# Kernel optimization log

Hardware: AMD Instinct MI355X
Metric: run time of the kernel (lower is better)

Reference implementation:

```python
import jax, jax.numpy as jnp
import numpy as np

B, N, L, H, V, OV, MAX_STEPS = 16, 256, 4, 128, 512, 1000, 48


def setup_inputs() -> dict:
    key = jax.random.key(0)
    ks = jax.random.split(key, 20)
    s = lambda fan_in: 1.0 / np.sqrt(fan_in)
    return {
        'data': jax.random.randint(ks[0], (B, N, L), 0, V, dtype=jnp.int32),
        'true_branch_nodes': jax.random.randint(ks[1], (B, N), 0, N, dtype=jnp.int32),
        'false_branch_nodes': jax.random.randint(ks[2], (B, N), 0, N, dtype=jnp.int32),
        'start_index': jax.random.randint(ks[3], (B,), 0, N, dtype=jnp.int32),
        'exit_index': jax.random.randint(ks[4], (B,), 0, N, dtype=jnp.int32),
        'steps': jax.random.randint(ks[5], (B,), 1, MAX_STEPS + 1, dtype=jnp.int32),
        'embed_w': jax.random.uniform(ks[6], (V, H), jnp.float32, -0.1, 0.1),
        'Wi0': jax.random.normal(ks[7], (H, 4 * H), jnp.float32) * s(H),
        'Wh0': jax.random.normal(ks[8], (H, 4 * H), jnp.float32) * s(H),
        'b0': jnp.zeros((4 * H,), jnp.float32),
        'Wi1': jax.random.normal(ks[9], (H, 4 * H), jnp.float32) * s(H),
        'Wh1': jax.random.normal(ks[10], (H, 4 * H), jnp.float32) * s(H),
        'b1': jnp.zeros((4 * H,), jnp.float32),
        'branch_w': jax.random.normal(ks[11], (4 * H, 2), jnp.float32) * s(4 * H),
        'branch_b': jax.random.normal(ks[12], (2,), jnp.float32) * 1e-6,
        'out_w': jax.random.normal(ks[13], (H, OV), jnp.float32) * s(H),
        'out_b': jax.random.normal(ks[14], (OV,), jnp.float32) * 1e-6,
    }


def _lstm(c, h, x, Wi, Wh, b):
    # flax LSTMCell gate order: i, f, g, o
    z = x @ Wi + h @ Wh + b
    i, f, g, o = jnp.split(z, 4, axis=-1)
    c = jax.nn.sigmoid(f) * c + jax.nn.sigmoid(i) * jnp.tanh(g)
    h = jax.nn.sigmoid(o) * jnp.tanh(c)
    return c, h


def reference(data, true_branch_nodes, false_branch_nodes, start_index, exit_index, steps,
              embed_w, Wi0, Wh0, b0, Wi1, Wh1, b1, branch_w, branch_b, out_w, out_b):
    num_nodes = data.shape[1]

    def single_example(data_e, true_idx, false_idx, start, exit_i, n_steps):
        emb_t = jnp.swapaxes(embed_w[data_e], 0, 1)  # [L, N, H]
        hs0 = tuple(jnp.zeros((num_nodes, H), embed_w.dtype) for _ in range(4))  # (c0,h0,c1,h1)
        ip0 = jnp.zeros((num_nodes,), embed_w.dtype).at[start].set(1.0)

        def execute(hs):
            # run 2-layer stacked LSTM over each node's statement tokens (vectorized over nodes)
            def tok_step(carry, x):
                c0, h0, c1, h1 = carry
                c0, h0 = _lstm(c0, h0, x, Wi0, Wh0, b0)
                c1, h1 = _lstm(c1, h1, h0, Wi1, Wh1, b1)
                return (c0, h0, c1, h1), None
            carry, _ = jax.lax.scan(tok_step, hs, emb_t)
            return carry

        def step(carry, idx):
            hs, ip = carry
            contrib = execute(hs)
            # exit node keeps its previous hidden state
            contrib = tuple(c.at[exit_i].set(h[exit_i]) for c, h in zip(contrib, hs))
            concat = jnp.concatenate(contrib, axis=-1)  # [N, 4H]
            p = jax.nn.softmax(concat @ branch_w + branch_b, axis=-1)
            pt, pf = p[:, 0], p[:, 1]
            wt, wf = pt * ip, pf * ip
            ip_new = (jax.ops.segment_sum(wt, true_idx, num_segments=num_nodes)
                      + jax.ops.segment_sum(wf, false_idx, num_segments=num_nodes))
            denom = (ip_new + 1e-7)[:, None]
            def agg(hleaf):
                t = jax.ops.segment_sum(hleaf * wt[:, None], true_idx, num_segments=num_nodes)
                f = jax.ops.segment_sum(hleaf * wf[:, None], false_idx, num_segments=num_nodes)
                return (t + f) / denom
            hs_new = tuple(agg(hleaf) for hleaf in contrib)
            active = idx < n_steps
            hs = tuple(jnp.where(active, new, old) for new, old in zip(hs_new, hs))
            ip = jnp.where(active, ip_new, ip)
            return (hs, ip), None

        (hs, ip), _ = jax.lax.scan(step, (hs0, ip0), jnp.arange(MAX_STEPS))
        return hs[3][exit_i] @ out_w + out_b  # top-layer h at exit node -> [OV]

    return jax.vmap(single_example)(data, true_branch_nodes, false_branch_nodes,
                                    start_index, exit_index, steps)
```

## Files before the change

### kernel.cpp

```cpp
#include <hip/hip_runtime.h>

namespace {
constexpr int B = 16, N = 256, L = 4, H = 128, V = 512, OV = 1000, MAX_STEPS = 48;
constexpr int Z = 4 * H;
constexpr int BN = B * N;
constexpr int PADK = 132;
}

typedef __attribute__((ext_vector_type(8))) short short8;
typedef __attribute__((ext_vector_type(4))) short short4v;
typedef __attribute__((ext_vector_type(4))) float f32x4;

__device__ __forceinline__ float sigf(float x) { return 1.0f / (1.0f + __expf(-x)); }
__device__ __forceinline__ float tanh_f(float x) { return 1.0f - 2.0f / (__expf(2.0f * x) + 1.0f); }

__device__ __forceinline__ unsigned short bf16_rne(float x) {
    unsigned u = __float_as_uint(x);
    return (unsigned short)((u + 0x7fffu + ((u >> 16) & 1u)) >> 16);
}
__device__ __forceinline__ void split2(float x, unsigned short& hi, unsigned short& lo) {
    hi = bf16_rne(x);
    const float hf = __uint_as_float(((unsigned)hi) << 16);
    lo = bf16_rne(x - hf);
}

__device__ __forceinline__ short8 ldsA(const unsigned short* p) {
    const short4v a = *(const short4v*)p;
    const short4v b = *(const short4v*)(p + 16);
    return __builtin_shufflevector(a, b, 0, 1, 2, 3, 4, 5, 6, 7);
}

__global__ __launch_bounds__(256) void k_init(float4* __restrict__ cur4,
                                              float* __restrict__ ip,
                                              const int* __restrict__ start) {
    const int idx = blockIdx.x * 256 + threadIdx.x;
    cur4[idx] = make_float4(0.f, 0.f, 0.f, 0.f);
    if (idx < BN) ip[idx] = ((idx & (N - 1)) == start[idx >> 8]) ? 1.0f : 0.0f;
}

__global__ __launch_bounds__(256) void k_tokz(const float* __restrict__ emb,
                                              const float* __restrict__ Wi0,
                                              const float* __restrict__ b0,
                                              float* __restrict__ tokz) {
    __shared__ float lds_a[16 * 128];
    float4* l4 = (float4*)lds_a;
    const int tid = threadIdx.x;
    const int c = tid & 127, rg = tid >> 7;
    const int row0 = blockIdx.x * 16;
    {
        const float4* a4 = (const float4*)emb;
        l4[tid] = a4[row0 * 32 + tid];
        l4[tid + 256] = a4[row0 * 32 + tid + 256];
    }
    __syncthreads();
    float acc[8][4];
    {
        float bq[4];
#pragma unroll
        for (int q = 0; q < 4; q++) bq[q] = b0[c + q * 128];
#pragma unroll
        for (int i = 0; i < 8; i++)
#pragma unroll
            for (int q = 0; q < 4; q++) acc[i][q] = bq[q];
    }
    for (int k4 = 0; k4 < 32; k4++) {
        float4 a[8];
#pragma unroll
        for (int i = 0; i < 8; i++) a[i] = l4[(rg * 8 + i) * 32 + k4];
#pragma unroll
        for (int j = 0; j < 4; j++) {
            const int k = k4 * 4 + j;
            const float* wr = Wi0 + k * Z + c;
            const float w0 = wr[0], w1 = wr[128], w2 = wr[256], w3 = wr[384];
#pragma unroll
            for (int i = 0; i < 8; i++) {
                const float av = (j == 0) ? a[i].x : (j == 1) ? a[i].y : (j == 2) ? a[i].z : a[i].w;
                acc[i][0] += av * w0;
                acc[i][1] += av * w1;
                acc[i][2] += av * w2;
                acc[i][3] += av * w3;
            }
        }
    }
#pragma unroll
    for (int i = 0; i < 8; i++) {
        const int row = row0 + rg * 8 + i;
#pragma unroll
        for (int q = 0; q < 4; q++) tokz[row * Z + c + q * 128] = acc[i][q];
    }
}

__global__ __launch_bounds__(256) void k_pack(const float* __restrict__ Wh0,
                                              const float* __restrict__ Wi1,
                                              const float* __restrict__ Wh1,
                                              unsigned short* __restrict__ WPhi,
                                              unsigned short* __restrict__ WPlo) {
    const int gid = blockIdx.x * 256 + threadIdx.x;
    const int lp = gid & 63;
    const int ks = (gid >> 6) & 3;
    const int w = (gid >> 8) & 7;
    const int q = (gid >> 11) & 3;
    const int split = (gid >> 13) & 1;
    const int mat = gid >> 14;
    const float* W = (mat == 0) ? Wh0 : (mat == 1) ? Wi1 : Wh1;
    const int g = lp >> 4, li = lp & 15;
    const int col = q * 128 + w * 16 + li;
    const int e = ((mat * 4 + q) * 8 + w) * 4 + ks;
    unsigned short* dst = (split ? WPlo : WPhi) + (size_t)e * 512 + lp * 8;
#pragma unroll
    for (int j = 0; j < 8; j++) {
        const int k = ks * 32 + ((j & 4) ? 16 : 0) + g * 4 + (j & 3);
        const float x = W[k * Z + col];
        const unsigned short hi = bf16_rne(x);
        unsigned short v = hi;
        if (split) {
            const float hf = __uint_as_float(((unsigned)hi) << 16);
            v = bf16_rne(x - hf);
        }
        dst[j] = v;
    }
}

__global__ __launch_bounds__(256) void k_csr(const int* __restrict__ tix,
                                             const int* __restrict__ fix,
                                             int* __restrict__ off,
                                             int* __restrict__ ent) {
    const int b = blockIdx.x;
    const int m = threadIdx.x;
    __shared__ int cnt[N];
    __shared__ int wsum[4];
    cnt[m] = 0;
    __syncthreads();
    const int ti = tix[b * N + m];
    const int fi = fix[b * N + m];
    atomicAdd(&cnt[ti], 1);
    atomicAdd(&cnt[fi], 1);
    __syncthreads();
    const int v = cnt[m];
    const int lane = m & 63, w = m >> 6;
    int sc = v;
#pragma unroll
    for (int o = 1; o < 64; o <<= 1) {
        const int t = __shfl_up(sc, o);
        if (lane >= o) sc += t;
    }
    if (lane == 63) wsum[w] = sc;
    __syncthreads();
    int add = 0;
    for (int i = 0; i < w; i++) add += wsum[i];
    const int base = sc - v + add;
    off[b * (N + 1) + m] = base;
    if (m == N - 1) off[b * (N + 1) + N] = base + v;
    __syncthreads();
    cnt[m] = base;
    __syncthreads();
    const int p1 = atomicAdd(&cnt[ti], 1);
    ent[b * 2 * N + p1] = (m << 1);
    const int p2 = atomicAdd(&cnt[fi], 1);
    ent[b * 2 * N + p2] = (m << 1) | 1;
}

__global__ __launch_bounds__(512) void k_scan(
    const float* __restrict__ c0c, const float* __restrict__ h0c,
    const float* __restrict__ c1c, const float* __restrict__ h1c,
    float* __restrict__ c0w, float* __restrict__ h0w,
    float* __restrict__ c1w, float* __restrict__ h1w,
    const unsigned short* __restrict__ WPhi, const unsigned short* __restrict__ WPlo,
    const float* __restrict__ b1,
    const float* __restrict__ tokz, const int* __restrict__ data,
    const float* __restrict__ bw, const float* __restrict__ bb,
    const float* __restrict__ ip, float* __restrict__ wt, float* __restrict__ wf,
    const int* __restrict__ exiti, const int* __restrict__ steps, const int s) {
    const int bx = blockIdx.x;
    const int b = bx >> 4;
    if (s >= steps[b]) return;
    const int row0 = bx * 16;
    const int tid = threadIdx.x;
    const int w = tid >> 6;
    const int l = tid & 63;
    const int g = l >> 4, li = l & 15;
    const int ch = w * 16 + li;

    __shared__ unsigned short h0hi[16 * PADK], h0lo[16 * PADK];
    __shared__ unsigned short h1hi[16 * PADK], h1lo[16 * PADK];
    __shared__ float red[16][8][2];

    float c0[4], c1[4], h0[4], h1[4];
#pragma unroll
    for (int r = 0; r < 4; r++) {
        const int off = (row0 + g * 4 + r) * H + ch;
        c0[r] = c0c[off];
        h0[r] = h0c[off];
        c1[r] = c1c[off];
        h1[r] = h1c[off];
    }
    float b1v[4];
#pragma unroll
    for (int q = 0; q < 4; q++) b1v[q] = b1[q * 128 + ch];

#pragma unroll
    for (int r = 0; r < 4; r++) {
        unsigned short hi, lo;
        split2(h0[r], hi, lo);
        h0hi[(g * 4 + r) * PADK + ch] = hi;
        h0lo[(g * 4 + r) * PADK + ch] = lo;
        split2(h1[r], hi, lo);
        h1hi[(g * 4 + r) * PADK + ch] = hi;
        h1lo[(g * 4 + r) * PADK + ch] = lo;
    }
    __syncthreads();

#pragma unroll 1
    for (int t = 0; t < L; t++) {
        f32x4 acc[4];
        {
            int tok[4];
#pragma unroll
            for (int r = 0; r < 4; r++) tok[r] = data[(row0 + g * 4 + r) * L + t];
#pragma unroll
            for (int q = 0; q < 4; q++)
#pragma unroll
                for (int r = 0; r < 4; r++) acc[q][r] = tokz[tok[r] * Z + q * 128 + ch];
        }
#pragma unroll
        for (int q = 0; q < 4; q++) {
#pragma unroll
            for (int ks = 0; ks < 4; ks++) {
                const int ab = li * PADK + ks * 32 + g * 4;
                const short8 ahi = ldsA(&h0hi[ab]);
                const short8 alo = ldsA(&h0lo[ab]);
                const int e = (q * 8 + w) * 4 + ks;
                const short8 bhi = *(const short8*)(WPhi + (size_t)e * 512 + l * 8);
                const short8 blo = *(const short8*)(WPlo + (size_t)e * 512 + l * 8);
                acc[q] = __builtin_amdgcn_mfma_f32_16x16x32_bf16(ahi, bhi, acc[q], 0, 0, 0);
                acc[q] = __builtin_amdgcn_mfma_f32_16x16x32_bf16(ahi, blo, acc[q], 0, 0, 0);
                acc[q] = __builtin_amdgcn_mfma_f32_16x16x32_bf16(alo, bhi, acc[q], 0, 0, 0);
            }
            __builtin_amdgcn_sched_barrier(0);
        }
#pragma unroll
        for (int r = 0; r < 4; r++) {
            const float cn = sigf(acc[1][r]) * c0[r] + sigf(acc[0][r]) * tanh_f(acc[2][r]);
            c0[r] = cn;
            h0[r] = sigf(acc[3][r]) * tanh_f(cn);
        }
        __syncthreads();
#pragma unroll
        for (int r = 0; r < 4; r++) {
            unsigned short hi, lo;
            split2(h0[r], hi, lo);
            h0hi[(g * 4 + r) * PADK + ch] = hi;
            h0lo[(g * 4 + r) * PADK + ch] = lo;
        }
        __syncthreads();
#pragma unroll
        for (int q = 0; q < 4; q++) {
            const float bv = b1v[q];
            acc[q][0] = bv; acc[q][1] = bv; acc[q][2] = bv; acc[q][3] = bv;
        }
#pragma unroll
        for (int q = 0; q < 4; q++) {
#pragma unroll
            for (int ks = 0; ks < 4; ks++) {
                const int ab = li * PADK + ks * 32 + g * 4;
                const short8 a0hi = ldsA(&h0hi[ab]);
                const short8 a0lo = ldsA(&h0lo[ab]);
                const short8 a1hi = ldsA(&h1hi[ab]);
                const short8 a1lo = ldsA(&h1lo[ab]);
                const int e1 = ((4 + q) * 8 + w) * 4 + ks;
                const int e2 = ((8 + q) * 8 + w) * 4 + ks;
                const short8 b1hi = *(const short8*)(WPhi + (size_t)e1 * 512 + l * 8);
                const short8 b1lo = *(const short8*)(WPlo + (size_t)e1 * 512 + l * 8);
                const short8 b2hi = *(const short8*)(WPhi + (size_t)e2 * 512 + l * 8);
                const short8 b2lo = *(const short8*)(WPlo + (size_t)e2 * 512 + l * 8);
                acc[q] = __builtin_amdgcn_mfma_f32_16x16x32_bf16(a0hi, b1hi, acc[q], 0, 0, 0);
                acc[q] = __builtin_amdgcn_mfma_f32_16x16x32_bf16(a0hi, b1lo, acc[q], 0, 0, 0);
                acc[q] = __builtin_amdgcn_mfma_f32_16x16x32_bf16(a0lo, b1hi, acc[q], 0, 0, 0);
                acc[q] = __builtin_amdgcn_mfma_f32_16x16x32_bf16(a1hi, b2hi, acc[q], 0, 0, 0);
                acc[q] = __builtin_amdgcn_mfma_f32_16x16x32_bf16(a1hi, b2lo, acc[q], 0, 0, 0);
                acc[q] = __builtin_amdgcn_mfma_f32_16x16x32_bf16(a1lo, b2hi, acc[q], 0, 0, 0);
            }
            __builtin_amdgcn_sched_barrier(0);
        }
#pragma unroll
        for (int r = 0; r < 4; r++) {
            const float cn = sigf(acc[1][r]) * c1[r] + sigf(acc[0][r]) * tanh_f(acc[2][r]);
            c1[r] = cn;
            h1[r] = sigf(acc[3][r]) * tanh_f(cn);
        }
        __syncthreads();
#pragma unroll
        for (int r = 0; r < 4; r++) {
            unsigned short hi, lo;
            split2(h1[r], hi, lo);
            h1hi[(g * 4 + r) * PADK + ch] = hi;
            h1lo[(g * 4 + r) * PADK + ch] = lo;
        }
        __syncthreads();
    }

    const int ex = exiti[b];
    if ((ex >> 4) == (bx & 15)) {
        const int rl = ex & 15;
#pragma unroll
        for (int r = 0; r < 4; r++) {
            if (g * 4 + r == rl) {
                const int off = (row0 + rl) * H + ch;
                c0[r] = c0c[off];
                h0[r] = h0c[off];
                c1[r] = c1c[off];
                h1[r] = h1c[off];
            }
        }
    }
#pragma unroll
    for (int r = 0; r < 4; r++) {
        const int off = (row0 + g * 4 + r) * H + ch;
        c0w[off] = c0[r];
        h0w[off] = h0[r];
        c1w[off] = c1[r];
        h1w[off] = h1[r];
    }
    float2 bwv[4];
#pragma unroll
    for (int x = 0; x < 4; x++) bwv[x] = ((const float2*)bw)[x * 128 + ch];
    float l0p[4], l1p[4];
#pragma unroll
    for (int r = 0; r < 4; r++) {
        l0p[r] = c0[r] * bwv[0].x + h0[r] * bwv[1].x + c1[r] * bwv[2].x + h1[r] * bwv[3].x;
        l1p[r] = c0[r] * bwv[0].y + h0[r] * bwv[1].y + c1[r] * bwv[2].y + h1[r] * bwv[3].y;
    }
#pragma unroll
    for (int off = 8; off > 0; off >>= 1)
#pragma unroll
        for (int r = 0; r < 4; r++) {
            l0p[r] += __shfl_xor(l0p[r], off);
            l1p[r] += __shfl_xor(l1p[r], off);
        }
    if (li == 0)
#pragma unroll
        for (int r = 0; r < 4; r++) {
            red[g * 4 + r][w][0] = l0p[r];
            red[g * 4 + r][w][1] = l1p[r];
        }
    __syncthreads();
    if (tid < 16) {
        float l0 = bb[0], l1 = bb[1];
#pragma unroll
        for (int ww = 0; ww < 8; ww++) {
            l0 += red[tid][ww][0];
            l1 += red[tid][ww][1];
        }
        const float m = fmaxf(l0, l1);
        const float e0 = __expf(l0 - m), e1 = __expf(l1 - m);
        const float inv = 1.0f / (e0 + e1);
        const float ipv = ip[row0 + tid];
        wt[row0 + tid] = e0 * inv * ipv;
        wf[row0 + tid] = e1 * inv * ipv;
    }
}

__global__ __launch_bounds__(256) void k_agg(
    const float* __restrict__ c0w, const float* __restrict__ h0w,
    const float* __restrict__ c1w, const float* __restrict__ h1w,
    float* __restrict__ c0c, float* __restrict__ h0c,
    float* __restrict__ c1c, float* __restrict__ h1c,
    const int* __restrict__ off, const int* __restrict__ ent,
    const float* __restrict__ wt, const float* __restrict__ wf,
    float* __restrict__ ip, const int* __restrict__ steps, const int s) {
    const int row00 = blockIdx.x * 4;
    const int b = row00 >> 8;
    if (s >= steps[b]) return;
    const int tid = threadIdx.x;
    const int lane = tid & 63;
    const int n = (row00 & (N - 1)) + (tid >> 6);
    const int rowb = b * N;
    const int beg = off[b * (N + 1) + n];
    const int end = off[b * (N + 1) + n + 1];
    float a00 = 0, a01 = 0, a10 = 0, a11 = 0, a20 = 0, a21 = 0, a30 = 0, a31 = 0;
    float ipacc = 0.f;
    for (int e = beg; e < end; e++) {
        const int pe = ent[b * 2 * N + e];
        const int m = pe >> 1;
        const float wgt = (pe & 1) ? wf[rowb + m] : wt[rowb + m];
        ipacc += wgt;
        const int rb = (rowb + m) * H;
        a00 += c0w[rb + lane] * wgt;
        a01 += c0w[rb + lane + 64] * wgt;
        a10 += h0w[rb + lane] * wgt;
        a11 += h0w[rb + lane + 64] * wgt;
        a20 += c1w[rb + lane] * wgt;
        a21 += c1w[rb + lane + 64] * wgt;
        a30 += h1w[rb + lane] * wgt;
        a31 += h1w[rb + lane + 64] * wgt;
    }
    const float dn = 1.0f / (ipacc + 1e-7f);
    const int ob = (rowb + n) * H;
    c0c[ob + lane] = a00 * dn;
    c0c[ob + lane + 64] = a01 * dn;
    h0c[ob + lane] = a10 * dn;
    h0c[ob + lane + 64] = a11 * dn;
    c1c[ob + lane] = a20 * dn;
    c1c[ob + lane + 64] = a21 * dn;
    h1c[ob + lane] = a30 * dn;
    h1c[ob + lane + 64] = a31 * dn;
    if (lane == 0) ip[rowb + n] = ipacc;
}

__global__ __launch_bounds__(256) void k_out(const float* __restrict__ h1c,
                                             const float* __restrict__ ow,
                                             const float* __restrict__ ob,
                                             const int* __restrict__ exiti,
                                             float* __restrict__ out) {
    const int b = blockIdx.x;
    __shared__ float h[H];
    const int tid = threadIdx.x;
    if (tid < H) h[tid] = h1c[(b * N + exiti[b]) * H + tid];
    __syncthreads();
    for (int v = tid; v < OV; v += 256) {
        float acc = ob[v];
        for (int d = 0; d < H; d++) acc += h[d] * ow[d * OV + v];
        out[b * OV + v] = acc;
    }
}

extern "C" void kernel_launch(void* const* d_in, const int* in_sizes, int n_in,
                              void* d_out, int out_size, void* d_ws, size_t ws_size,
                              hipStream_t stream) {
    (void)in_sizes; (void)n_in; (void)out_size;
    const int* data = (const int*)d_in[0];
    const int* tix = (const int*)d_in[1];
    const int* fix = (const int*)d_in[2];
    const int* start = (const int*)d_in[3];
    const int* exiti = (const int*)d_in[4];
    const int* steps = (const int*)d_in[5];
    const float* emb = (const float*)d_in[6];
    const float* Wi0 = (const float*)d_in[7];
    const float* Wh0 = (const float*)d_in[8];
    const float* b0 = (const float*)d_in[9];
    const float* Wi1 = (const float*)d_in[10];
    const float* Wh1 = (const float*)d_in[11];
    const float* b1 = (const float*)d_in[12];
    const float* bw = (const float*)d_in[13];
    const float* bb = (const float*)d_in[14];
    const float* ow = (const float*)d_in[15];
    const float* obias = (const float*)d_in[16];
    float* out = (float*)d_out;

    const size_t SB = (size_t)BN * H;
    float* ws = (float*)d_ws;
    float* c0c = ws;
    float* h0c = ws + 1 * SB;
    float* c1c = ws + 2 * SB;
    float* h1c = ws + 3 * SB;
    float* c0w = ws + 4 * SB;
    float* h0w = ws + 5 * SB;
    float* c1w = ws + 6 * SB;
    float* h1w = ws + 7 * SB;
    float* tokz = ws + 8 * SB;
    float* ip = tokz + (size_t)V * Z;
    float* wt = ip + BN;
    float* wf = wt + BN;
    unsigned short* WPhi = (unsigned short*)(wf + BN);
    unsigned short* WPlo = WPhi + 3 * 65536;
    int* csr_off = (int*)(WPlo + 3 * 65536);
    int* csr_ent = csr_off + B * (N + 1);
    const size_t need = (8 * SB + (size_t)V * Z + 3 * (size_t)BN) * sizeof(float) +
                        2 * 3 * 65536 * sizeof(unsigned short) +
                        (B * (N + 1) + B * 2 * N) * sizeof(int);
    if (ws_size < need) return;

    k_init<<<(4 * SB / 4) / 256, 256, 0, stream>>>((float4*)ws, ip, start);
    k_tokz<<<V / 16, 256, 0, stream>>>(emb, Wi0, b0, tokz);
    k_pack<<<192, 256, 0, stream>>>(Wh0, Wi1, Wh1, WPhi, WPlo);
    k_csr<<<B, 256, 0, stream>>>(tix, fix, csr_off, csr_ent);

    for (int s = 0; s < MAX_STEPS; s++) {
        k_scan<<<BN / 16, 512, 0, stream>>>(c0c, h0c, c1c, h1c, c0w, h0w, c1w, h1w,
                                            WPhi, WPlo, b1, tokz, data, bw, bb,
                                            ip, wt, wf, exiti, steps, s);
        k_agg<<<BN / 4, 256, 0, stream>>>(c0w, h0w, c1w, h1w, c0c, h0c, c1c, h1c,
                                          csr_off, csr_ent, wt, wf, ip, steps, s);
    }
    k_out<<<B, 256, 0, stream>>>(h1c, ow, obias, exiti, out);
}
```

Baseline: 4.658 ms.

## Fuse segment-sum aggregation into scan kernel with ping-pong work buffers

Removes the separate aggregation and init kernels. Each scan block now gathers its 16 nodes' state from the previous step's ping-pong buffer into LDS, so the current state never round-trips through global memory. The launch count drops from 96 to 49 and the exit-node restore is taken from registers instead of a reload. The trade-offs are a larger LDS footprint per block, which may lower occupancy, and an extra launch at s==MAX_STEPS that writes the final h1.

```diff
diff --git a/kernel.cpp b/kernel.cpp
--- a/kernel.cpp
+++ b/kernel.cpp
@@ -5,6 +5,7 @@
 constexpr int Z = 4 * H;
 constexpr int BN = B * N;
 constexpr int PADK = 132;
+constexpr size_t SB = (size_t)BN * H;
 }
 
 typedef __attribute__((ext_vector_type(8))) short short8;
@@ -28,14 +29,6 @@
     const short4v a = *(const short4v*)p;
     const short4v b = *(const short4v*)(p + 16);
     return __builtin_shufflevector(a, b, 0, 1, 2, 3, 4, 5, 6, 7);
-}
-
-__global__ __launch_bounds__(256) void k_init(float4* __restrict__ cur4,
-                                              float* __restrict__ ip,
-                                              const int* __restrict__ start) {
-    const int idx = blockIdx.x * 256 + threadIdx.x;
-    cur4[idx] = make_float4(0.f, 0.f, 0.f, 0.f);
-    if (idx < BN) ip[idx] = ((idx & (N - 1)) == start[idx >> 8]) ? 1.0f : 0.0f;
 }
 
 __global__ __launch_bounds__(256) void k_tokz(const float* __restrict__ emb,
@@ -161,19 +154,22 @@
 }
 
 __global__ __launch_bounds__(512) void k_scan(
-    const float* __restrict__ c0c, const float* __restrict__ h0c,
-    const float* __restrict__ c1c, const float* __restrict__ h1c,
-    float* __restrict__ c0w, float* __restrict__ h0w,
-    float* __restrict__ c1w, float* __restrict__ h1w,
+    const float* __restrict__ workR,
+    float* __restrict__ workW,
+    const float* __restrict__ wtR, const float* __restrict__ wfR,
+    float* __restrict__ wtW, float* __restrict__ wfW,
+    float* __restrict__ h1c,
     const unsigned short* __restrict__ WPhi, const unsigned short* __restrict__ WPlo,
     const float* __restrict__ b1,
     const float* __restrict__ tokz, const int* __restrict__ data,
     const float* __restrict__ bw, const float* __restrict__ bb,
-    const float* __restrict__ ip, float* __restrict__ wt, float* __restrict__ wf,
-    const int* __restrict__ exiti, const int* __restrict__ steps, const int s) {
+    const int* __restrict__ csr_off, const int* __restrict__ csr_ent,
+    const int* __restrict__ start, const int* __restrict__ exiti,
+    const int* __restrict__ steps, const int s) {
     const int bx = blockIdx.x;
     const int b = bx >> 4;
-    if (s >= steps[b]) return;
+    const int st = steps[b];
+    if (s > st) return;
     const int row0 = bx * 16;
     const int tid = threadIdx.x;
     const int w = tid >> 6;
@@ -184,16 +180,72 @@
     __shared__ unsigned short h0hi[16 * PADK], h0lo[16 * PADK];
     __shared__ unsigned short h1hi[16 * PADK], h1lo[16 * PADK];
     __shared__ float red[16][8][2];
+    __shared__ float curt[4][16][132];
+    __shared__ float ipl[16];
+
+    if (s == 0) {
+        for (int i = tid; i < 4 * 16 * 132; i += 512) (&curt[0][0][0])[i] = 0.f;
+        if (tid < 16) ipl[tid] = ((bx & 15) * 16 + tid == start[b]) ? 1.0f : 0.0f;
+    } else {
+#pragma unroll 1
+        for (int rr = 0; rr < 2; rr++) {
+            const int nloc = w * 2 + rr;
+            const int n = (bx & 15) * 16 + nloc;
+            const int beg = csr_off[b * (N + 1) + n];
+            const int end = csr_off[b * (N + 1) + n + 1];
+            float a00 = 0, a01 = 0, a10 = 0, a11 = 0, a20 = 0, a21 = 0, a30 = 0, a31 = 0;
+            float ipacc = 0.f;
+            for (int e = beg; e < end; e++) {
+                const int pe = csr_ent[b * 2 * N + e];
+                const int m = pe >> 1;
+                const float wgt = (pe & 1) ? wfR[b * N + m] : wtR[b * N + m];
+                ipacc += wgt;
+                const size_t rb = (size_t)(b * N + m) * H;
+                a00 += workR[rb + l] * wgt;
+                a01 += workR[rb + l + 64] * wgt;
+                a10 += workR[SB + rb + l] * wgt;
+                a11 += workR[SB + rb + l + 64] * wgt;
+                a20 += workR[2 * SB + rb + l] * wgt;
+                a21 += workR[2 * SB + rb + l + 64] * wgt;
+                a30 += workR[3 * SB + rb + l] * wgt;
+                a31 += workR[3 * SB + rb + l + 64] * wgt;
+            }
+            const float dn = 1.0f / (ipacc + 1e-7f);
+            curt[0][nloc][l] = a00 * dn;
+            curt[0][nloc][l + 64] = a01 * dn;
+            curt[1][nloc][l] = a10 * dn;
+            curt[1][nloc][l + 64] = a11 * dn;
+            curt[2][nloc][l] = a20 * dn;
+            curt[2][nloc][l + 64] = a21 * dn;
+            curt[3][nloc][l] = a30 * dn;
+            curt[3][nloc][l + 64] = a31 * dn;
+            if (l == 0) ipl[nloc] = ipacc;
+        }
+    }
+    __syncthreads();
 
     float c0[4], c1[4], h0[4], h1[4];
 #pragma unroll
     for (int r = 0; r < 4; r++) {
-        const int off = (row0 + g * 4 + r) * H + ch;
-        c0[r] = c0c[off];
-        h0[r] = h0c[off];
-        c1[r] = c1c[off];
-        h1[r] = h1c[off];
-    }
+        const int rl = g * 4 + r;
+        c0[r] = curt[0][rl][ch];
+        h0[r] = curt[1][rl][ch];
+        c1[r] = curt[2][rl][ch];
+        h1[r] = curt[3][rl][ch];
+    }
+
+    if (s == st) {
+#pragma unroll
+        for (int r = 0; r < 4; r++) h1c[(size_t)(row0 + g * 4 + r) * H + ch] = h1[r];
+        return;
+    }
+
+    const int ex = exiti[b];
+    int rex = -1;
+    if ((ex >> 4) == (bx & 15) && ((ex & 15) >> 2) == g) rex = ex & 3;
+    float sc0 = 0, sh0 = 0, sc1 = 0, sh1 = 0;
+    if (rex >= 0) { sc0 = c0[rex]; sh0 = h0[rex]; sc1 = c1[rex]; sh1 = h1[rex]; }
+
     float b1v[4];
 #pragma unroll
     for (int q = 0; q < 4; q++) b1v[q] = b1[q * 128 + ch];
@@ -299,27 +351,14 @@
         __syncthreads();
     }
 
-    const int ex = exiti[b];
-    if ((ex >> 4) == (bx & 15)) {
-        const int rl = ex & 15;
-#pragma unroll
-        for (int r = 0; r < 4; r++) {
-            if (g * 4 + r == rl) {
-                const int off = (row0 + rl) * H + ch;
-                c0[r] = c0c[off];
-                h0[r] = h0c[off];
-                c1[r] = c1c[off];
-                h1[r] = h1c[off];
-            }
-        }
-    }
+    if (rex >= 0) { c0[rex] = sc0; h0[rex] = sh0; c1[rex] = sc1; h1[rex] = sh1; }
 #pragma unroll
     for (int r = 0; r < 4; r++) {
-        const int off = (row0 + g * 4 + r) * H + ch;
-        c0w[off] = c0[r];
-        h0w[off] = h0[r];
-        c1w[off] = c1[r];
-        h1w[off] = h1[r];
+        const size_t off = (size_t)(row0 + g * 4 + r) * H + ch;
+        workW[off] = c0[r];
+        workW[SB + off] = h0[r];
+        workW[2 * SB + off] = c1[r];
+        workW[3 * SB + off] = h1[r];
     }
     float2 bwv[4];
 #pragma unroll
@@ -354,57 +393,10 @@
         const float m = fmaxf(l0, l1);
         const float e0 = __expf(l0 - m), e1 = __expf(l1 - m);
         const float inv = 1.0f / (e0 + e1);
-        const float ipv = ip[row0 + tid];
-        wt[row0 + tid] = e0 * inv * ipv;
-        wf[row0 + tid] = e1 * inv * ipv;
-    }
-}
-
-__global__ __launch_bounds__(256) void k_agg(
-    const float* __restrict__ c0w, const float* __restrict__ h0w,
-    const float* __restrict__ c1w, const float* __restrict__ h1w,
-    float* __restrict__ c0c, float* __restrict__ h0c,
-    float* __restrict__ c1c, float* __restrict__ h1c,
-    const int* __restrict__ off, const int* __restrict__ ent,
-    const float* __restrict__ wt, const float* __restrict__ wf,
-    float* __restrict__ ip, const int* __restrict__ steps, const int s) {
-    const int row00 = blockIdx.x * 4;
-    const int b = row00 >> 8;
-    if (s >= steps[b]) return;
-    const int tid = threadIdx.x;
-    const int lane = tid & 63;
-    const int n = (row00 & (N - 1)) + (tid >> 6);
-    const int rowb = b * N;
-    const int beg = off[b * (N + 1) + n];
-    const int end = off[b * (N + 1) + n + 1];
-    float a00 = 0, a01 = 0, a10 = 0, a11 = 0, a20 = 0, a21 = 0, a30 = 0, a31 = 0;
-    float ipacc = 0.f;
-    for (int e = beg; e < end; e++) {
-        const int pe = ent[b * 2 * N + e];
-        const int m = pe >> 1;
-        const float wgt = (pe & 1) ? wf[rowb + m] : wt[rowb + m];
-        ipacc += wgt;
-        const int rb = (rowb + m) * H;
-        a00 += c0w[rb + lane] * wgt;
-        a01 += c0w[rb + lane + 64] * wgt;
-        a10 += h0w[rb + lane] * wgt;
-        a11 += h0w[rb + lane + 64] * wgt;
-        a20 += c1w[rb + lane] * wgt;
-        a21 += c1w[rb + lane + 64] * wgt;
-        a30 += h1w[rb + lane] * wgt;
-        a31 += h1w[rb + lane + 64] * wgt;
-    }
-    const float dn = 1.0f / (ipacc + 1e-7f);
-    const int ob = (rowb + n) * H;
-    c0c[ob + lane] = a00 * dn;
-    c0c[ob + lane + 64] = a01 * dn;
-    h0c[ob + lane] = a10 * dn;
-    h0c[ob + lane + 64] = a11 * dn;
-    c1c[ob + lane] = a20 * dn;
-    c1c[ob + lane + 64] = a21 * dn;
-    h1c[ob + lane] = a30 * dn;
-    h1c[ob + lane + 64] = a31 * dn;
-    if (lane == 0) ip[rowb + n] = ipacc;
+        const float ipv = ipl[tid];
+        wtW[row0 + tid] = e0 * inv * ipv;
+        wfW[row0 + tid] = e1 * inv * ipv;
+    }
 }
 
 __global__ __launch_bounds__(256) void k_out(const float* __restrict__ h1c,
@@ -415,7 +407,7 @@
     const int b = blockIdx.x;
     __shared__ float h[H];
     const int tid = threadIdx.x;
-    if (tid < H) h[tid] = h1c[(b * N + exiti[b]) * H + tid];
+    if (tid < H) h[tid] = h1c[(size_t)(b * N + exiti[b]) * H + tid];
     __syncthreads();
     for (int v = tid; v < OV; v += 256) {
         float acc = ob[v];
@@ -447,40 +439,38 @@
     const float* obias = (const float*)d_in[16];
     float* out = (float*)d_out;
 
-    const size_t SB = (size_t)BN * H;
     float* ws = (float*)d_ws;
-    float* c0c = ws;
-    float* h0c = ws + 1 * SB;
-    float* c1c = ws + 2 * SB;
-    float* h1c = ws + 3 * SB;
-    float* c0w = ws + 4 * SB;
-    float* h0w = ws + 5 * SB;
-    float* c1w = ws + 6 * SB;
-    float* h1w = ws + 7 * SB;
-    float* tokz = ws + 8 * SB;
-    float* ip = tokz + (size_t)V * Z;
-    float* wt = ip + BN;
-    float* wf = wt + BN;
-    unsigned short* WPhi = (unsigned short*)(wf + BN);
+    float* tokz = ws;
+    float* work0 = tokz + (size_t)V * Z;
+    float* work1 = work0 + 4 * SB;
+    float* wt0 = work1 + 4 * SB;
+    float* wf0 = wt0 + BN;
+    float* wt1 = wf0 + BN;
+    float* wf1 = wt1 + BN;
+    float* h1c = wf1 + BN;
+    unsigned short* WPhi = (unsigned short*)(h1c + SB);
     unsigned short* WPlo = WPhi + 3 * 65536;
     int* csr_off = (int*)(WPlo + 3 * 65536);
     int* csr_ent = csr_off + B * (N + 1);
-    const size_t need = (8 * SB + (size_t)V * Z + 3 * (size_t)BN) * sizeof(float) +
+    const size_t need = ((size_t)V * Z + 9 * SB + 4 * (size_t)BN) * sizeof(float) +
                         2 * 3 * 65536 * sizeof(unsigned short) +
                         (B * (N + 1) + B * 2 * N) * sizeof(int);
     if (ws_size < need) return;
 
-    k_init<<<(4 * SB / 4) / 256, 256, 0, stream>>>((float4*)ws, ip, start);
     k_tokz<<<V / 16, 256, 0, stream>>>(emb, Wi0, b0, tokz);
     k_pack<<<192, 256, 0, stream>>>(Wh0, Wi1, Wh1, WPhi, WPlo);
     k_csr<<<B, 256, 0, stream>>>(tix, fix, csr_off, csr_ent);
 
-    for (int s = 0; s < MAX_STEPS; s++) {
-        k_scan<<<BN / 16, 512, 0, stream>>>(c0c, h0c, c1c, h1c, c0w, h0w, c1w, h1w,
+    for (int s = 0; s <= MAX_STEPS; s++) {
+        float* workW = (s & 1) ? work1 : work0;
+        const float* workR = (s & 1) ? work0 : work1;
+        float* wtW = (s & 1) ? wt1 : wt0;
+        float* wfW = (s & 1) ? wf1 : wf0;
+        const float* wtR = (s & 1) ? wt0 : wt1;
+        const float* wfR = (s & 1) ? wf0 : wf1;
+        k_scan<<<BN / 16, 512, 0, stream>>>(workR, workW, wtR, wfR, wtW, wfW, h1c,
                                             WPhi, WPlo, b1, tokz, data, bw, bb,
-                                            ip, wt, wf, exiti, steps, s);
-        k_agg<<<BN / 4, 256, 0, stream>>>(c0w, h0w, c1w, h1w, c0c, h0c, c1c, h1c,
-                                          csr_off, csr_ent, wt, wf, ip, steps, s);
+                                            csr_off, csr_ent, start, exiti, steps, s);
     }
     k_out<<<B, 256, 0, stream>>>(h1c, ow, obias, exiti, out);
 }
```

After: 4.819 ms, median of 2. 3.4% more time.

## Process 32 rows per scan block to reuse weight fragments across two MFMA tiles

Applied to the files above, without the earlier changes.

Each k_scan block now handles 32 node rows as two 16-row MFMA tiles, so every weight fragment loaded from global memory feeds two sets of MFMAs. This halves weight traffic per row and halves the block count to 128. Weight loads also switch to nontemporal loads. The trade-offs are fewer blocks on a many-CU GPU, roughly double the accumulator registers, and more shared memory per block.

```diff
diff --git a/kernel.cpp b/kernel.cpp
--- a/kernel.cpp
+++ b/kernel.cpp
@@ -28,6 +28,9 @@
     const short4v a = *(const short4v*)p;
     const short4v b = *(const short4v*)(p + 16);
     return __builtin_shufflevector(a, b, 0, 1, 2, 3, 4, 5, 6, 7);
+}
+__device__ __forceinline__ short8 ldw(const unsigned short* p) {
+    return __builtin_nontemporal_load((const short8*)p);
 }
 
 __global__ __launch_bounds__(256) void k_init(float4* __restrict__ cur4,
@@ -172,179 +175,218 @@
     const float* __restrict__ ip, float* __restrict__ wt, float* __restrict__ wf,
     const int* __restrict__ exiti, const int* __restrict__ steps, const int s) {
     const int bx = blockIdx.x;
-    const int b = bx >> 4;
+    const int b = bx >> 3;
     if (s >= steps[b]) return;
-    const int row0 = bx * 16;
+    const int row0 = bx * 32;
     const int tid = threadIdx.x;
     const int w = tid >> 6;
     const int l = tid & 63;
     const int g = l >> 4, li = l & 15;
     const int ch = w * 16 + li;
 
-    __shared__ unsigned short h0hi[16 * PADK], h0lo[16 * PADK];
-    __shared__ unsigned short h1hi[16 * PADK], h1lo[16 * PADK];
-    __shared__ float red[16][8][2];
-
-    float c0[4], c1[4], h0[4], h1[4];
-#pragma unroll
-    for (int r = 0; r < 4; r++) {
-        const int off = (row0 + g * 4 + r) * H + ch;
-        c0[r] = c0c[off];
-        h0[r] = h0c[off];
-        c1[r] = c1c[off];
-        h1[r] = h1c[off];
-    }
+    __shared__ unsigned short h0hi[32 * PADK], h0lo[32 * PADK];
+    __shared__ unsigned short h1hi[32 * PADK], h1lo[32 * PADK];
+    __shared__ float red[32][8][2];
+
+    float c0[2][4], c1[2][4], h0[2][4], h1[2][4];
+#pragma unroll
+    for (int u = 0; u < 2; u++)
+#pragma unroll
+        for (int r = 0; r < 4; r++) {
+            const int off = (row0 + u * 16 + g * 4 + r) * H + ch;
+            c0[u][r] = c0c[off];
+            h0[u][r] = h0c[off];
+            c1[u][r] = c1c[off];
+            h1[u][r] = h1c[off];
+        }
     float b1v[4];
 #pragma unroll
     for (int q = 0; q < 4; q++) b1v[q] = b1[q * 128 + ch];
 
 #pragma unroll
-    for (int r = 0; r < 4; r++) {
-        unsigned short hi, lo;
-        split2(h0[r], hi, lo);
-        h0hi[(g * 4 + r) * PADK + ch] = hi;
-        h0lo[(g * 4 + r) * PADK + ch] = lo;
-        split2(h1[r], hi, lo);
-        h1hi[(g * 4 + r) * PADK + ch] = hi;
-        h1lo[(g * 4 + r) * PADK + ch] = lo;
-    }
+    for (int u = 0; u < 2; u++)
+#pragma unroll
+        for (int r = 0; r < 4; r++) {
+            const int rl = u * 16 + g * 4 + r;
+            unsigned short hi, lo;
+            split2(h0[u][r], hi, lo);
+            h0hi[rl * PADK + ch] = hi;
+            h0lo[rl * PADK + ch] = lo;
+            split2(h1[u][r], hi, lo);
+            h1hi[rl * PADK + ch] = hi;
+            h1lo[rl * PADK + ch] = lo;
+        }
     __syncthreads();
 
 #pragma unroll 1
     for (int t = 0; t < L; t++) {
-        f32x4 acc[4];
+        f32x4 acc[4][2];
         {
-            int tok[4];
-#pragma unroll
-            for (int r = 0; r < 4; r++) tok[r] = data[(row0 + g * 4 + r) * L + t];
+            int tok[2][4];
+#pragma unroll
+            for (int u = 0; u < 2; u++)
+#pragma unroll
+                for (int r = 0; r < 4; r++)
+                    tok[u][r] = data[(row0 + u * 16 + g * 4 + r) * L + t];
 #pragma unroll
             for (int q = 0; q < 4; q++)
 #pragma unroll
-                for (int r = 0; r < 4; r++) acc[q][r] = tokz[tok[r] * Z + q * 128 + ch];
+                for (int u = 0; u < 2; u++)
+#pragma unroll
+                    for (int r = 0; r < 4; r++)
+                        acc[q][u][r] = tokz[tok[u][r] * Z + q * 128 + ch];
         }
 #pragma unroll
         for (int q = 0; q < 4; q++) {
 #pragma unroll
             for (int ks = 0; ks < 4; ks++) {
-                const int ab = li * PADK + ks * 32 + g * 4;
-                const short8 ahi = ldsA(&h0hi[ab]);
-                const short8 alo = ldsA(&h0lo[ab]);
                 const int e = (q * 8 + w) * 4 + ks;
-                const short8 bhi = *(const short8*)(WPhi + (size_t)e * 512 + l * 8);
-                const short8 blo = *(const short8*)(WPlo + (size_t)e * 512 + l * 8);
-                acc[q] = __builtin_amdgcn_mfma_f32_16x16x32_bf16(ahi, bhi, acc[q], 0, 0, 0);
-                acc[q] = __builtin_amdgcn_mfma_f32_16x16x32_bf16(ahi, blo, acc[q], 0, 0, 0);
-                acc[q] = __builtin_amdgcn_mfma_f32_16x16x32_bf16(alo, bhi, acc[q], 0, 0, 0);
+                const short8 bhi = ldw(WPhi + (size_t)e * 512 + l * 8);
+                const short8 blo = ldw(WPlo + (size_t)e * 512 + l * 8);
+#pragma unroll
+                for (int u = 0; u < 2; u++) {
+                    const int ab = (u * 16 + li) * PADK + ks * 32 + g * 4;
+                    const short8 ahi = ldsA(&h0hi[ab]);
+                    const short8 alo = ldsA(&h0lo[ab]);
+                    acc[q][u] = __builtin_amdgcn_mfma_f32_16x16x32_bf16(ahi, bhi, acc[q][u], 0, 0, 0);
+                    acc[q][u] = __builtin_amdgcn_mfma_f32_16x16x32_bf16(ahi, blo, acc[q][u], 0, 0, 0);
+                    acc[q][u] = __builtin_amdgcn_mfma_f32_16x16x32_bf16(alo, bhi, acc[q][u], 0, 0, 0);
+                }
             }
             __builtin_amdgcn_sched_barrier(0);
         }
 #pragma unroll
-        for (int r = 0; r < 4; r++) {
-            const float cn = sigf(acc[1][r]) * c0[r] + sigf(acc[0][r]) * tanh_f(acc[2][r]);
-            c0[r] = cn;
-            h0[r] = sigf(acc[3][r]) * tanh_f(cn);
-        }
+        for (int u = 0; u < 2; u++)
+#pragma unroll
+            for (int r = 0; r < 4; r++) {
+                const float cn = sigf(acc[1][u][r]) * c0[u][r] + sigf(acc[0][u][r]) * tanh_f(acc[2][u][r]);
+                c0[u][r] = cn;
+                h0[u][r] = sigf(acc[3][u][r]) * tanh_f(cn);
+            }
         __syncthreads();
 #pragma unroll
-        for (int r = 0; r < 4; r++) {
-            unsigned short hi, lo;
-            split2(h0[r], hi, lo);
-            h0hi[(g * 4 + r) * PADK + ch] = hi;
-            h0lo[(g * 4 + r) * PADK + ch] = lo;
-        }
+        for (int u = 0; u < 2; u++)
+#pragma unroll
+            for (int r = 0; r < 4; r++) {
+                const int rl = u * 16 + g * 4 + r;
+                unsigned short hi, lo;
+                split2(h0[u][r], hi, lo);
+                h0hi[rl * PADK + ch] = hi;
+                h0lo[rl * PADK + ch] = lo;
+            }
         __syncthreads();
 #pragma unroll
+        for (int q = 0; q < 4; q++)
+#pragma unroll
+            for (int u = 0; u < 2; u++) {
+                const float bv = b1v[q];
+                acc[q][u][0] = bv; acc[q][u][1] = bv; acc[q][u][2] = bv; acc[q][u][3] = bv;
+            }
+#pragma unroll
         for (int q = 0; q < 4; q++) {
-            const float bv = b1v[q];
-            acc[q][0] = bv; acc[q][1] = bv; acc[q][2] = bv; acc[q][3] = bv;
-        }
-#pragma unroll
-        for (int q = 0; q < 4; q++) {
 #pragma unroll
             for (int ks = 0; ks < 4; ks++) {
-                const int ab = li * PADK + ks * 32 + g * 4;
-                const short8 a0hi = ldsA(&h0hi[ab]);
-                const short8 a0lo = ldsA(&h0lo[ab]);
-                const short8 a1hi = ldsA(&h1hi[ab]);
-                const short8 a1lo = ldsA(&h1lo[ab]);
                 const int e1 = ((4 + q) * 8 + w) * 4 + ks;
                 const int e2 = ((8 + q) * 8 + w) * 4 + ks;
-                const short8 b1hi = *(const short8*)(WPhi + (size_t)e1 * 512 + l * 8);
-                const short8 b1lo = *(const short8*)(WPlo + (size_t)e1 * 512 + l * 8);
-                const short8 b2hi = *(const short8*)(WPhi + (size_t)e2 * 512 + l * 8);
-                const short8 b2lo = *(const short8*)(WPlo + (size_t)e2 * 512 + l * 8);
-                acc[q] = __builtin_amdgcn_mfma_f32_16x16x32_bf16(a0hi, b1hi, acc[q], 0, 0, 0);
-                acc[q] = __builtin_amdgcn_mfma_f32_16x16x32_bf16(a0hi, b1lo, acc[q], 0, 0, 0);
-                acc[q] = __builtin_amdgcn_mfma_f32_16x16x32_bf16(a0lo, b1hi, acc[q], 0, 0, 0);
-                acc[q] = __builtin_amdgcn_mfma_f32_16x16x32_bf16(a1hi, b2hi, acc[q], 0, 0, 0);
-                acc[q] = __builtin_amdgcn_mfma_f32_16x16x32_bf16(a1hi, b2lo, acc[q], 0, 0, 0);
-                acc[q] = __builtin_amdgcn_mfma_f32_16x16x32_bf16(a1lo, b2hi, acc[q], 0, 0, 0);
+                const short8 b1hi = ldw(WPhi + (size_t)e1 * 512 + l * 8);
+                const short8 b1lo = ldw(WPlo + (size_t)e1 * 512 + l * 8);
+                const short8 b2hi = ldw(WPhi + (size_t)e2 * 512 + l * 8);
+                const short8 b2lo = ldw(WPlo + (size_t)e2 * 512 + l * 8);
+#pragma unroll
+                for (int u = 0; u < 2; u++) {
+                    const int ab = (u * 16 + li) * PADK + ks * 32 + g * 4;
+                    const short8 a0hi = ldsA(&h0hi[ab]);
+                    const short8 a0lo = ldsA(&h0lo[ab]);
+                    const short8 a1hi = ldsA(&h1hi[ab]);
+                    const short8 a1lo = ldsA(&h1lo[ab]);
+                    acc[q][u] = __builtin_amdgcn_mfma_f32_16x16x32_bf16(a0hi, b1hi, acc[q][u], 0, 0, 0);
+                    acc[q][u] = __builtin_amdgcn_mfma_f32_16x16x32_bf16(a0hi, b1lo, acc[q][u], 0, 0, 0);
+                    acc[q][u] = __builtin_amdgcn_mfma_f32_16x16x32_bf16(a0lo, b1hi, acc[q][u], 0, 0, 0);
+                    acc[q][u] = __builtin_amdgcn_mfma_f32_16x16x32_bf16(a1hi, b2hi, acc[q][u], 0, 0, 0);
+                    acc[q][u] = __builtin_amdgcn_mfma_f32_16x16x32_bf16(a1hi, b2lo, acc[q][u], 0, 0, 0);
+                    acc[q][u] = __builtin_amdgcn_mfma_f32_16x16x32_bf16(a1lo, b2hi, acc[q][u], 0, 0, 0);
+                }
             }
             __builtin_amdgcn_sched_barrier(0);
         }
 #pragma unroll
+        for (int u = 0; u < 2; u++)
+#pragma unroll
+            for (int r = 0; r < 4; r++) {
+                const float cn = sigf(acc[1][u][r]) * c1[u][r] + sigf(acc[0][u][r]) * tanh_f(acc[2][u][r]);
+                c1[u][r] = cn;
+                h1[u][r] = sigf(acc[3][u][r]) * tanh_f(cn);
+            }
+        __syncthreads();
+#pragma unroll
+        for (int u = 0; u < 2; u++)
+#pragma unroll
+            for (int r = 0; r < 4; r++) {
+                const int rl = u * 16 + g * 4 + r;
+                unsigned short hi, lo;
+                split2(h1[u][r], hi, lo);
+                h1hi[rl * PADK + ch] = hi;
+                h1lo[rl * PADK + ch] = lo;
+            }
+        __syncthreads();
+    }
+
+    const int ex = exiti[b];
+    if ((ex >> 5) == (bx & 7)) {
+        const int rl = ex & 31;
+#pragma unroll
+        for (int u = 0; u < 2; u++)
+#pragma unroll
+            for (int r = 0; r < 4; r++) {
+                if (u * 16 + g * 4 + r == rl) {
+                    const int off = (row0 + rl) * H + ch;
+                    c0[u][r] = c0c[off];
+                    h0[u][r] = h0c[off];
+                    c1[u][r] = c1c[off];
+                    h1[u][r] = h1c[off];
+                }
+            }
+    }
+#pragma unroll
+    for (int u = 0; u < 2; u++)
+#pragma unroll
         for (int r = 0; r < 4; r++) {
-            const float cn = sigf(acc[1][r]) * c1[r] + sigf(acc[0][r]) * tanh_f(acc[2][r]);
-            c1[r] = cn;
-            h1[r] = sigf(acc[3][r]) * tanh_f(cn);
-        }
-        __syncthreads();
+            const int off = (row0 + u * 16 + g * 4 + r) * H + ch;
+            c0w[off] = c0[u][r];
+            h0w[off] = h0[u][r];
+            c1w[off] = c1[u][r];
+            h1w[off] = h1[u][r];
+        }
+    float2 bwv[4];
+#pragma unroll
+    for (int x = 0; x < 4; x++) bwv[x] = ((const float2*)bw)[x * 128 + ch];
+    float l0p[2][4], l1p[2][4];
+#pragma unroll
+    for (int u = 0; u < 2; u++)
 #pragma unroll
         for (int r = 0; r < 4; r++) {
-            unsigned short hi, lo;
-            split2(h1[r], hi, lo);
-            h1hi[(g * 4 + r) * PADK + ch] = hi;
-            h1lo[(g * 4 + r) * PADK + ch] = lo;
-        }
-        __syncthreads();
-    }
-
-    const int ex = exiti[b];
-    if ((ex >> 4) == (bx & 15)) {
-        const int rl = ex & 15;
-#pragma unroll
-        for (int r = 0; r < 4; r++) {
-            if (g * 4 + r == rl) {
-                const int off = (row0 + rl) * H + ch;
-                c0[r] = c0c[off];
-                h0[r] = h0c[off];
-                c1[r] = c1c[off];
-                h1[r] = h1c[off];
-            }
-        }
-    }
-#pragma unroll
-    for (int r = 0; r < 4; r++) {
-        const int off = (row0 + g * 4 + r) * H + ch;
-        c0w[off] = c0[r];
-        h0w[off] = h0[r];
-        c1w[off] = c1[r];
-        h1w[off] = h1[r];
-    }
-    float2 bwv[4];
-#pragma unroll
-    for (int x = 0; x < 4; x++) bwv[x] = ((const float2*)bw)[x * 128 + ch];
-    float l0p[4], l1p[4];
-#pragma unroll
-    for (int r = 0; r < 4; r++) {
-        l0p[r] = c0[r] * bwv[0].x + h0[r] * bwv[1].x + c1[r] * bwv[2].x + h1[r] * bwv[3].x;
-        l1p[r] = c0[r] * bwv[0].y + h0[r] * bwv[1].y + c1[r] * bwv[2].y + h1[r] * bwv[3].y;
-    }
+            l0p[u][r] = c0[u][r] * bwv[0].x + h0[u][r] * bwv[1].x + c1[u][r] * bwv[2].x + h1[u][r] * bwv[3].x;
+            l1p[u][r] = c0[u][r] * bwv[0].y + h0[u][r] * bwv[1].y + c1[u][r] * bwv[2].y + h1[u][r] * bwv[3].y;
+        }
 #pragma unroll
     for (int off = 8; off > 0; off >>= 1)
 #pragma unroll
-        for (int r = 0; r < 4; r++) {
-            l0p[r] += __shfl_xor(l0p[r], off);
-            l1p[r] += __shfl_xor(l1p[r], off);
-        }
+        for (int u = 0; u < 2; u++)
+#pragma unroll
+            for (int r = 0; r < 4; r++) {
+                l0p[u][r] += __shfl_xor(l0p[u][r], off);
+                l1p[u][r] += __shfl_xor(l1p[u][r], off);
+            }
     if (li == 0)
 #pragma unroll
-        for (int r = 0; r < 4; r++) {
-            red[g * 4 + r][w][0] = l0p[r];
-            red[g * 4 + r][w][1] = l1p[r];
-        }
-    __syncthreads();
-    if (tid < 16) {
+        for (int u = 0; u < 2; u++)
+#pragma unroll
+            for (int r = 0; r < 4; r++) {
+                red[u * 16 + g * 4 + r][w][0] = l0p[u][r];
+                red[u * 16 + g * 4 + r][w][1] = l1p[u][r];
+            }
+    __syncthreads();
+    if (tid < 32) {
         float l0 = bb[0], l1 = bb[1];
 #pragma unroll
         for (int ww = 0; ww < 8; ww++) {
@@ -476,7 +518,7 @@
     k_csr<<<B, 256, 0, stream>>>(tix, fix, csr_off, csr_ent);
 
     for (int s = 0; s < MAX_STEPS; s++) {
-        k_scan<<<BN / 16, 512, 0, stream>>>(c0c, h0c, c1c, h1c, c0w, h0w, c1w, h1w,
+        k_scan<<<BN / 32, 512, 0, stream>>>(c0c, h0c, c1c, h1c, c0w, h0w, c1w, h1w,
                                             WPhi, WPlo, b1, tokz, data, bw, bb,
                                             ip, wt, wf, exiti, steps, s);
         k_agg<<<BN / 4, 256, 0, stream>>>(c0w, h0w, c1w, h1w, c0c, h0c, c1c, h1c,
```

Result: slower. 6.152 ms (+32.1%).
